# Optimization experiments

Hardware: AMD Instinct MI355X
Metric: run time of the kernel (lower is better)

The kernel has to match this reference:

```python
import jax, jax.numpy as jnp
import numpy as np
from jax import lax

EPS = 1e-5
COMMIT_W = 0.25

def conv2d(x, w, b):
    # x: [N,C,H,W], w: [O,I,3,3], SAME padding, stride 1
    y = lax.conv_general_dilated(x, w, (1, 1), 'SAME',
                                 dimension_numbers=('NCHW', 'OIHW', 'NCHW'))
    return y + b[None, :, None, None]

def batchnorm(x, gamma, beta):
    # training-mode batch norm over (N,H,W)
    m = jnp.mean(x, axis=(0, 2, 3), keepdims=True)
    v = jnp.var(x, axis=(0, 2, 3), keepdims=True)
    xhat = (x - m) * lax.rsqrt(v + EPS)
    return xhat * gamma[None, :, None, None] + beta[None, :, None, None]

def maxpool2(x):
    return lax.reduce_window(x, -jnp.inf, lax.max, (1, 1, 2, 2), (1, 1, 2, 2), 'VALID')

def setup_inputs() -> dict:
    key = jax.random.key(0)
    ks = jax.random.split(key, 8)
    B, C, H, W, D, K = 8, 3, 256, 256, 64, 1024
    return {
        'x': jax.random.normal(ks[0], (B, C, H, W), jnp.float32),
        'conv1_w': jax.random.normal(ks[1], (D, C, 3, 3), jnp.float32) * 0.05,
        'conv1_b': jnp.zeros((D,), jnp.float32),
        'bn1_gamma': jnp.ones((D,), jnp.float32),
        'bn1_beta': jnp.zeros((D,), jnp.float32),
        'embed': jax.random.normal(ks[2], (K, D), jnp.float32),
        'conv2_w': jax.random.normal(ks[3], (C, D, 3, 3), jnp.float32) * 0.05,
        'conv2_b': jnp.zeros((C,), jnp.float32),
        'bn2_gamma': jnp.ones((C,), jnp.float32),
        'bn2_beta': jnp.zeros((C,), jnp.float32),
    }

def reference(x, conv1_w, conv1_b, bn1_gamma, bn1_beta, embed,
              conv2_w, conv2_b, bn2_gamma, bn2_beta):
    # ---- encoder ----
    h = conv2d(x, conv1_w, conv1_b)
    h = batchnorm(h, bn1_gamma, bn1_beta)
    h = jax.nn.relu(h)
    h = maxpool2(h)                      # [B, D, H/2, W/2]
    B, D, Hh, Wh = h.shape
    # ---- vector quantize (accept_image_fmap) ----
    flat = jnp.transpose(h, (0, 2, 3, 1)).reshape(-1, D)   # [N, D]
    # squared euclidean distance to each code
    dist = (jnp.sum(flat * flat, axis=1, keepdims=True)
            - 2.0 * flat @ embed.T
            + jnp.sum(embed * embed, axis=1)[None, :])     # [N, K]
    idx = jnp.argmin(dist, axis=1)                          # [N]
    quant = embed[idx]                                      # gather [N, D]
    commit_loss = COMMIT_W * jnp.mean((lax.stop_gradient(quant) - flat) ** 2)
    # straight-through estimator
    quant_st = flat + lax.stop_gradient(quant - flat)
    q = jnp.transpose(quant_st.reshape(B, Hh, Wh, D), (0, 3, 1, 2))  # [B,D,Hh,Wh]
    indices = idx.reshape(B, Hh, Wh)
    # ---- decoder ----
    up = jnp.repeat(jnp.repeat(q, 2, axis=2), 2, axis=3)    # nearest x2
    y = conv2d(up, conv2_w, conv2_b)
    y = batchnorm(y, bn2_gamma, bn2_beta)
    y = jnp.tanh(y)
    return (y, indices, commit_loss)
```

## Files before the change

### kernel.cpp

```cpp
#include <hip/hip_runtime.h>
#include <hip/hip_bf16.h>
#include <math.h>

typedef unsigned int u32;
typedef unsigned short u16;
typedef __attribute__((ext_vector_type(8))) short short8v;
typedef __attribute__((ext_vector_type(4))) float f32x4;

#define HH 256
#define WW 256
#define HP 128
#define WP 128
#define NPTS (8*HP*WP)
#define NPIX 524288
#define Y_ELEMS (8*3*HH*WW)
#define IDX_OFF Y_ELEMS
#define LOSS_OFF (Y_ELEMS + NPTS)
#define MARGIN_MFMA 0.05f

__device__ __forceinline__ u32 bfr(float f) {
  u32 u = __float_as_uint(f);
  return (u + 0x7FFFu + ((u >> 16) & 1u)) >> 16;
}
__device__ __forceinline__ float bff(u32 h) { return __uint_as_float(h << 16); }

__global__ __launch_bounds__(256) void k1_fused(
    const float* __restrict__ x, const float* __restrict__ w1,
    const float* __restrict__ b1, double* __restrict__ part1,
    float* __restrict__ pooled) {
  __shared__ float wl[27*64];
  __shared__ float b1s[64];
  __shared__ float xs[3][4][68];
  __shared__ double sred[4][128];
  int t = threadIdx.x;
  for (int i = t; i < 27*64; i += 256) { int c = i & 63; int tap = i >> 6; wl[i] = w1[c*27 + tap]; }
  if (t < 64) b1s[t] = b1[t];
  int bx = blockIdx.x;
  int b = bx >> 9;
  int pid0 = (bx & 511) * 32;
  int py = pid0 >> 7;
  int px0 = pid0 & 127;
  int gcol0 = 2*px0 - 1, grow0 = 2*py - 1;
  for (int i = t; i < 816; i += 256) {
    int j = i % 68;
    int rr = (i / 68) & 3;
    int ic = i / 272;
    int col = gcol0 + j, row = grow0 + rr;
    float v = 0.f;
    if (col >= 0 && col < WW && row >= 0 && row < HH)
      v = x[((size_t)((b*3 + ic)*HH + row))*WW + col];
    xs[ic][rr][j] = v;
  }
  __syncthreads();
  int lpx = t >> 3;
  int co = (t & 7) * 8;
  float A0[8], A1[8], C0[8], C1[8];
  #pragma unroll
  for (int c = 0; c < 8; ++c) { float bb = b1s[co + c]; A0[c] = bb; A1[c] = bb; C0[c] = bb; C1[c] = bb; }
  #pragma unroll
  for (int ic = 0; ic < 3; ++ic) {
    #pragma unroll
    for (int dy = 0; dy < 3; ++dy) {
      const float* wb = wl + (size_t)((ic*3 + dy)*3)*64 + co;
      int j0 = 2*lpx;
      float xa0 = xs[ic][dy][j0+0], xa1 = xs[ic][dy][j0+1], xa2 = xs[ic][dy][j0+2], xa3 = xs[ic][dy][j0+3];
      float xc0 = xs[ic][dy+1][j0+0], xc1 = xs[ic][dy+1][j0+1], xc2 = xs[ic][dy+1][j0+2], xc3 = xs[ic][dy+1][j0+3];
      #pragma unroll
      for (int c = 0; c < 8; ++c) {
        float w0 = wb[c], w1v = wb[64 + c], w2v = wb[128 + c];
        A0[c] = fmaf(xa0, w0, fmaf(xa1, w1v, fmaf(xa2, w2v, A0[c])));
        A1[c] = fmaf(xa1, w0, fmaf(xa2, w1v, fmaf(xa3, w2v, A1[c])));
        C0[c] = fmaf(xc0, w0, fmaf(xc1, w1v, fmaf(xc2, w2v, C0[c])));
        C1[c] = fmaf(xc1, w0, fmaf(xc2, w1v, fmaf(xc3, w2v, C1[c])));
      }
    }
  }
  double s[8], q[8];
  float m[8];
  #pragma unroll
  for (int c = 0; c < 8; ++c) {
    double dA0 = (double)A0[c], dA1 = (double)A1[c], dC0 = (double)C0[c], dC1 = (double)C1[c];
    double s_ = 0.0;
    s_ += dA0 + dA1;
    double q_ = fma(dA0, dA0, 0.0);
    q_ = fma(dA1, dA1, q_);
    float m_ = fmaxf(-3.4e38f, fmaxf(A0[c], A1[c]));
    s_ += dC0 + dC1;
    q_ = fma(dC0, dC0, q_);
    q_ = fma(dC1, dC1, q_);
    m_ = fmaxf(m_, fmaxf(C0[c], C1[c]));
    s[c] = s_; q[c] = q_; m[c] = m_;
  }
  int pid = pid0 + lpx;
  size_t p = (size_t)b*16384 + pid;
  *(float4*)(pooled + p*64 + co)     = make_float4(m[0], m[1], m[2], m[3]);
  *(float4*)(pooled + p*64 + co + 4) = make_float4(m[4], m[5], m[6], m[7]);
  #pragma unroll 1
  for (int c = 0; c < 8; ++c) {
    #pragma unroll
    for (int st = 8; st < 64; st <<= 1) {
      s[c] += __shfl_xor(s[c], st, 64);
      q[c] += __shfl_xor(q[c], st, 64);
    }
  }
  int w = t >> 6;
  if ((t & 63) < 8) {
    #pragma unroll
    for (int c = 0; c < 8; ++c) {
      sred[w][co + c] = s[c];
      sred[w][64 + co + c] = q[c];
    }
  }
  __syncthreads();
  if (t < 128)
    part1[(size_t)bx*128 + t] = (sred[0][t] + sred[1][t]) + (sred[2][t] + sred[3][t]);
}

__global__ __launch_bounds__(256) void k2_reduce_bn1(
    const double* __restrict__ part1, const float* __restrict__ gamma,
    const float* __restrict__ beta, double* __restrict__ sAB1,
    const float* __restrict__ w2, float* __restrict__ weff) {
  int bx = blockIdx.x;
  if (bx >= 64) {
    int e = (bx - 64)*256 + threadIdx.x;
    int oc = e & 3;
    int ic = (e >> 2) & 63;
    int combo = e >> 8;
    if (oc == 3) { weff[e] = 0.f; return; }
    int bq = combo & 1, a = (combo >> 1) & 1, ex = (combo >> 2) & 1, ey = combo >> 3;
    int rs = (a == 0) ? 0 : (ey == 0 ? 1 : 2);
    int rc = ((a ^ ey) != 0) ? 2 : 1;
    int cs = (bq == 0) ? 0 : (ex == 0 ? 1 : 2);
    int cc = ((bq ^ ex) != 0) ? 2 : 1;
    float ssum = 0.f;
    for (int i = 0; i < rc; ++i)
      for (int j = 0; j < cc; ++j)
        ssum += w2[((oc*64 + ic)*3 + (rs + i))*3 + (cs + j)];
    weff[e] = ssum;
    return;
  }
  int c = bx, t = threadIdx.x;
  double s = 0.0, q = 0.0;
  for (int i = t; i < 4096; i += 256) {
    const double* p = part1 + (size_t)i*128;
    s += p[c];
    q += p[64 + c];
  }
  __shared__ double ls[256], lq[256];
  ls[t] = s; lq[t] = q;
  __syncthreads();
  for (int o = 128; o > 0; o >>= 1) {
    if (t < o) { ls[t] += ls[t+o]; lq[t] += lq[t+o]; }
    __syncthreads();
  }
  if (t == 0) {
    double mean = ls[0] / (double)NPIX;
    double var  = lq[0] / (double)NPIX - mean*mean;
    double A = (double)gamma[c] / sqrt(var + 1e-5);
    sAB1[c] = A;
    sAB1[64 + c] = (double)beta[c] - mean*A;
  }
}

__global__ void kE_prep(const float* __restrict__ embed, char* __restrict__ epack,
                        double* __restrict__ enormd, float* __restrict__ enf,
                        u32* __restrict__ flagcnt,
                        const float* __restrict__ weff, float* __restrict__ proj) {
  int bxx = blockIdx.x;
  if (bxx >= 4) {
    int e = (bxx - 4)*256 + threadIdx.x;
    int k = e >> 6;
    int slot = e & 63;
    int combo = slot >> 2, oc = slot & 3;
    if (oc == 3) { proj[e] = 0.f; return; }
    const float* er = embed + (size_t)k*64;
    const float* wc = weff + combo*256 + oc;
    float s0 = 0.f, s1 = 0.f;
    #pragma unroll 8
    for (int ic = 0; ic < 64; ic += 2) {
      s0 = fmaf(er[ic],     wc[ic*4],     s0);
      s1 = fmaf(er[ic + 1], wc[ic*4 + 4], s1);
    }
    proj[e] = s0 + s1;
    return;
  }
  if (bxx == 0 && threadIdx.x == 0) flagcnt[0] = 0u;
  int k = bxx*256 + threadIdx.x;
  const float4* e4 = (const float4*)(embed + (size_t)k*64);
  u32 hw[32], lw[32];
  double s0 = 0.0, s1 = 0.0;
  #pragma unroll
  for (int i = 0; i < 16; ++i) {
    float4 v = e4[i];
    float f0 = v.x, f1 = v.y, f2 = v.z, f3 = v.w;
    s0 = fma((double)f0, (double)f0, s0); s1 = fma((double)f1, (double)f1, s1);
    s0 = fma((double)f2, (double)f2, s0); s1 = fma((double)f3, (double)f3, s1);
    u32 h0 = bfr(f0), h1 = bfr(f1), h2 = bfr(f2), h3 = bfr(f3);
    u32 l0 = bfr(f0 - bff(h0)), l1 = bfr(f1 - bff(h1));
    u32 l2 = bfr(f2 - bff(h2)), l3 = bfr(f3 - bff(h3));
    hw[2*i]   = h0 | (h1 << 16);
    hw[2*i+1] = h2 | (h3 << 16);
    lw[2*i]   = l0 | (l1 << 16);
    lw[2*i+1] = l2 | (l3 << 16);
  }
  char* tb = epack + (size_t)(k >> 4)*4096 + (size_t)(k & 15)*16;
  #pragma unroll
  for (int g = 0; g < 4; ++g) {
    *(uint4*)(tb + 0*1024 + g*256) = make_uint4(hw[4*g+0], hw[4*g+1], hw[4*g+2], hw[4*g+3]);
    *(uint4*)(tb + 1*1024 + g*256) = make_uint4(hw[16+4*g+0], hw[16+4*g+1], hw[16+4*g+2], hw[16+4*g+3]);
    *(uint4*)(tb + 2*1024 + g*256) = make_uint4(lw[4*g+0], lw[4*g+1], lw[4*g+2], lw[4*g+3]);
    *(uint4*)(tb + 3*1024 + g*256) = make_uint4(lw[16+4*g+0], lw[16+4*g+1], lw[16+4*g+2], lw[16+4*g+3]);
  }
  double e = s0 + s1;
  enormd[k] = e;
  enf[k] = (float)e;
}

#define MFMA_BF16 __builtin_amdgcn_mfma_f32_16x16x32_bf16
#define PROC_T(ntv) { \
  int code = (ntv)*16 + col; \
  float en2 = senf[code];    \
  f32x4 accA0={en2,en2,en2,en2}, accA1={0.f,0.f,0.f,0.f}; \
  f32x4 accB0={en2,en2,en2,en2}, accB1={0.f,0.f,0.f,0.f}; \
  __builtin_amdgcn_s_setprio(1); \
  accA0 = MFMA_BF16(aA_h0, b_h0, accA0, 0, 0, 0); \
  accA1 = MFMA_BF16(aA_h1, b_h1, accA1, 0, 0, 0); \
  accB0 = MFMA_BF16(aB_h0, b_h0, accB0, 0, 0, 0); \
  accB1 = MFMA_BF16(aB_h1, b_h1, accB1, 0, 0, 0); \
  accA0 = MFMA_BF16(aA_l0, b_h0, accA0, 0, 0, 0); \
  accA1 = MFMA_BF16(aA_l1, b_h1, accA1, 0, 0, 0); \
  accB0 = MFMA_BF16(aB_l0, b_h0, accB0, 0, 0, 0); \
  accB1 = MFMA_BF16(aB_l1, b_h1, accB1, 0, 0, 0); \
  accA0 = MFMA_BF16(aA_h0, b_l0, accA0, 0, 0, 0); \
  accA1 = MFMA_BF16(aA_h1, b_l1, accA1, 0, 0, 0); \
  accB0 = MFMA_BF16(aB_h0, b_l0, accB0, 0, 0, 0); \
  accB1 = MFMA_BF16(aB_h1, b_l1, accB1, 0, 0, 0); \
  __builtin_amdgcn_s_setprio(0); \
  _Pragma("unroll") \
  for (int j = 0; j < 4; ++j) { \
    float mA = accA0[j] + accA1[j]; \
    bool cA = mA > bestA[j]; \
    b2A[j] = __builtin_amdgcn_fmed3f(b2A[j], mA, bestA[j]);   \
    bestA[j] = fmaxf(bestA[j], mA); \
    idxA[j] = cA ? code : idxA[j]; \
    float mB = accB0[j] + accB1[j]; \
    bool cB = mB > bestB[j]; \
    b2B[j] = __builtin_amdgcn_fmed3f(b2B[j], mB, bestB[j]); \
    bestB[j] = fmaxf(bestB[j], mB); \
    idxB[j] = cB ? code : idxB[j]; \
  } \
}
#define PROC_LDS(bb, ntv) { \
  short8v b_h0 = *(const short8v*)((bb) + 0*1024 + lane*16); \
  short8v b_h1 = *(const short8v*)((bb) + 1*1024 + lane*16); \
  short8v b_l0 = *(const short8v*)((bb) + 2*1024 + lane*16); \
  short8v b_l1 = *(const short8v*)((bb) + 3*1024 + lane*16); \
  PROC_T(ntv); \
}

__global__ __launch_bounds__(256) void kB_mfma(
    const float* __restrict__ pooled, const double* __restrict__ sAB1,
    const char* __restrict__ epack, const float* __restrict__ enf,
    int* __restrict__ idxbuf, float* __restrict__ out_f, double* __restrict__ lossq,
    u32* __restrict__ flagcnt, u32* __restrict__ flagids) {
  __shared__ float senf[1024];
  __shared__ char shbuf[32768];
  __shared__ float fnp[256];
  __shared__ float fnsum[128];
  __shared__ float sAs[64], sBs[64];
  __shared__ double wred[4];
  int t = threadIdx.x;
  for (int i = t; i < 1024; i += 256) senf[i] = -0.5f * enf[i];
  if (t < 64) { sAs[t] = (float)sAB1[t]; sBs[t] = (float)sAB1[64 + t]; }
  __syncthreads();
  {
    int lp = t >> 1, h = t & 1, cb = h*32;
    int p = blockIdx.x*128 + lp;
    const float4* src = (const float4*)(pooled + (size_t)p*64 + cb);
    float fn = 0.f;
    u32 hw[16], lw[16];
    #pragma unroll
    for (int i = 0; i < 8; ++i) {
      float4 v = src[i];
      float f0 = fmaxf(fmaf(v.x, sAs[cb+4*i+0], sBs[cb+4*i+0]), 0.f);
      float f1 = fmaxf(fmaf(v.y, sAs[cb+4*i+1], sBs[cb+4*i+1]), 0.f);
      float f2 = fmaxf(fmaf(v.z, sAs[cb+4*i+2], sBs[cb+4*i+2]), 0.f);
      float f3 = fmaxf(fmaf(v.w, sAs[cb+4*i+3], sBs[cb+4*i+3]), 0.f);
      fn = fmaf(f0, f0, fn); fn = fmaf(f1, f1, fn);
      fn = fmaf(f2, f2, fn); fn = fmaf(f3, f3, fn);
      u32 h0 = bfr(f0), h1 = bfr(f1), h2 = bfr(f2), h3 = bfr(f3);
      u32 l0 = bfr(f0 - bff(h0)), l1 = bfr(f1 - bff(h1));
      u32 l2 = bfr(f2 - bff(h2)), l3 = bfr(f3 - bff(h3));
      hw[2*i]   = h0 | (h1 << 16);
      hw[2*i+1] = h2 | (h3 << 16);
      lw[2*i]   = l0 | (l1 << 16);
      lw[2*i+1] = l2 | (l3 << 16);
    }
    uint4* dh = (uint4*)(shbuf + (size_t)lp*256 + h*64);
    uint4* dl = (uint4*)(shbuf + (size_t)lp*256 + 128 + h*64);
    #pragma unroll
    for (int i = 0; i < 4; ++i) dh[i] = make_uint4(hw[4*i], hw[4*i+1], hw[4*i+2], hw[4*i+3]);
    #pragma unroll
    for (int i = 0; i < 4; ++i) dl[i] = make_uint4(lw[4*i], lw[4*i+1], lw[4*i+2], lw[4*i+3]);
    fnp[t] = fn;
  }
  __syncthreads();
  if ((t & 1) == 0) fnsum[t >> 1] = fnp[t] + fnp[t + 1];
  int lane = t & 63;
  int col = lane & 15, g = lane >> 4;
  int w = t >> 6;
  const char* fbA = shbuf + (size_t)(w*32 + col)*256 + 16*g;
  const char* fbB = shbuf + (size_t)(w*32 + 16 + col)*256 + 16*g;
  short8v aA_h0 = *(const short8v*)(fbA);
  short8v aA_h1 = *(const short8v*)(fbA + 64);
  short8v aA_l0 = *(const short8v*)(fbA + 128);
  short8v aA_l1 = *(const short8v*)(fbA + 192);
  short8v aB_h0 = *(const short8v*)(fbB);
  short8v aB_h1 = *(const short8v*)(fbB + 64);
  short8v aB_l0 = *(const short8v*)(fbB + 128);
  short8v aB_l1 = *(const short8v*)(fbB + 192);
  __syncthreads();
  char (*btile)[4][4096] = (char (*)[4][4096])shbuf;
  float bestA[4], b2A[4], bestB[4], b2B[4];
  int idxA[4], idxB[4];
  #pragma unroll
  for (int j = 0; j < 4; ++j) {
    bestA[j] = -3.4e38f; b2A[j] = -3.4e38f; idxA[j] = 0;
    bestB[j] = -3.4e38f; b2B[j] = -3.4e38f; idxB[j] = 0;
  }
  #pragma unroll
  for (int k = 0; k < 4; ++k)
    *(uint4*)(&btile[0][k][t*16]) = *(const uint4*)(epack + (size_t)k*4096 + (size_t)t*16);
  __syncthreads();
  #pragma unroll 1
  for (int ng = 0; ng < 16; ++ng) {
    int cur = ng & 1;
    uint4 stg0, stg1, stg2, stg3;
    if (ng < 15) {
      const char* base = epack + (size_t)(4*ng + 4)*4096 + (size_t)t*16;
      stg0 = *(const uint4*)(base);
      stg1 = *(const uint4*)(base + 4096);
      stg2 = *(const uint4*)(base + 8192);
      stg3 = *(const uint4*)(base + 12288);
    }
    PROC_LDS(&btile[cur][0][0], 4*ng + 0);
    PROC_LDS(&btile[cur][1][0], 4*ng + 1);
    PROC_LDS(&btile[cur][2][0], 4*ng + 2);
    PROC_LDS(&btile[cur][3][0], 4*ng + 3);
    if (ng < 15) {
      *(uint4*)(&btile[cur ^ 1][0][t*16]) = stg0;
      *(uint4*)(&btile[cur ^ 1][1][t*16]) = stg1;
      *(uint4*)(&btile[cur ^ 1][2][t*16]) = stg2;
      *(uint4*)(&btile[cur ^ 1][3][t*16]) = stg3;
    }
    __syncthreads();
  }
  double lsum = 0.0;
  #pragma unroll
  for (int grp = 0; grp < 2; ++grp) {
    #pragma unroll
    for (int j = 0; j < 4; ++j) {
      float b  = (grp == 0) ? bestA[j] : bestB[j];
      float s2 = (grp == 0) ? b2A[j]   : b2B[j];
      int  id  = (grp == 0) ? idxA[j]  : idxB[j];
      #pragma unroll
      for (int m = 1; m < 16; m <<= 1) {
        float ob  = __shfl_xor(b, m, 64);
        float os2 = __shfl_xor(s2, m, 64);
        int  oid  = __shfl_xor(id, m, 64);
        s2 = fmaxf(fmaxf(s2, os2), fminf(b, ob));
        if (ob > b || (ob == b && oid < id)) { b = ob; id = oid; }
      }
      if (col == 0) {
        int lpt = w*32 + grp*16 + g*4 + j;
        int p = blockIdx.x*128 + lpt;
        idxbuf[p] = id;
        out_f[IDX_OFF + p] = (float)id;
        lsum += (double)fmaf(-2.f, b, fnsum[lpt]);
        if (b - s2 <= 0.5f*MARGIN_MFMA) { u32 pos = atomicAdd(flagcnt, 1u); flagids[pos] = (u32)p; }
      }
    }
  }
  #pragma unroll
  for (int m = 1; m < 64; m <<= 1) lsum += __shfl_xor(lsum, m, 64);
  if (lane == 0) wred[w] = lsum;
  __syncthreads();
  if (t == 0) lossq[blockIdx.x] = (wred[0] + wred[1]) + (wred[2] + wred[3]);
}

__global__ __launch_bounds__(64) void kC_fallback(
    const float* __restrict__ x, const float* __restrict__ w1,
    const float* __restrict__ b1, const double* __restrict__ sAB1,
    const float* __restrict__ embed, const double* __restrict__ enormd,
    const u32* __restrict__ flagcnt, const u32* __restrict__ flagids,
    int* __restrict__ idxbuf, float* __restrict__ out_f,
    const double* __restrict__ lossq) {
  int lane = threadIdx.x;
  if (blockIdx.x == gridDim.x - 1) {
    double s = 0.0;
    for (int i = lane; i < 1024; i += 64) s += lossq[i];
    #pragma unroll
    for (int st = 1; st < 64; st <<= 1) s += __shfl_xor(s, st, 64);
    if (lane == 0) out_f[LOSS_OFF] = (float)(0.25 * s / (double)((size_t)NPTS * 64));
    return;
  }
  __shared__ double fd[64];
  double wv[27];
  #pragma unroll
  for (int i = 0; i < 27; ++i) wv[i] = (double)w1[lane*27 + i];
  double bias = (double)b1[lane];
  double A = sAB1[lane], B = sAB1[64 + lane];
  u32 n = flagcnt[0];
  u32 stride = gridDim.x - 1;
  for (u32 i = blockIdx.x; i < n; i += stride) {
    int p = (int)flagids[i];
    int b = p >> 14, py = (p >> 7) & 127, px = p & 127;
    double mx = -1e300;
    #pragma unroll
    for (int ry = 0; ry < 2; ++ry) {
      #pragma unroll
      for (int cx = 0; cx < 2; ++cx) {
        double a = bias;
        int yy = 2*py + ry, xx = 2*px + cx;
        #pragma unroll
        for (int ic = 0; ic < 3; ++ic) {
          #pragma unroll
          for (int dy = 0; dy < 3; ++dy) {
            int ryy = yy + dy - 1;
            if (ryy >= 0 && ryy < HH) {
              const float* row = x + ((size_t)((b*3 + ic)*HH + ryy))*WW;
              #pragma unroll
              for (int dxx = 0; dxx < 3; ++dxx) {
                int xc = xx + dxx - 1;
                if (xc >= 0 && xc < WW) a = fma((double)row[xc], wv[(ic*3 + dy)*3 + dxx], a);
              }
            }
          }
        }
        mx = fmax(mx, a);
      }
    }
    fd[lane] = fmax(fma(mx, A, B), 0.0);
    __syncthreads();
    double bd = 1e300; int bk = 1 << 20;
    for (int kk = 0; kk < 16; ++kk) {
      int k = kk*64 + lane;
      const float* e = embed + (size_t)k*64;
      double e0=0,e1=0,e2=0,e3=0;
      #pragma unroll
      for (int d = 0; d < 16; ++d) {
        e0 = fma(fd[4*d+0], (double)e[4*d+0], e0);
        e1 = fma(fd[4*d+1], (double)e[4*d+1], e1);
        e2 = fma(fd[4*d+2], (double)e[4*d+2], e2);
        e3 = fma(fd[4*d+3], (double)e[4*d+3], e3);
      }
      double dist = fma(-2.0, (e0+e1)+(e2+e3), enormd[k]);
      if (dist < bd) { bd = dist; bk = k; }
    }
    #pragma unroll
    for (int st = 1; st < 64; st <<= 1) {
      double od = __shfl_xor(bd, st, 64);
      int ok = __shfl_xor(bk, st, 64);
      if (od < bd || (od == bd && ok < bk)) { bd = od; bk = ok; }
    }
    if (lane == 0) {
      idxbuf[p] = bk;
      out_f[IDX_OFF + p] = (float)bk;
    }
    __syncthreads();
  }
}

template<int MODE>
__global__ __launch_bounds__(256) void conv2_body(
    const int* __restrict__ idxbuf, const float* __restrict__ proj,
    const float* __restrict__ c2b, const float* __restrict__ sAB2,
    float* __restrict__ part2, float* __restrict__ ybuf, float* __restrict__ yout) {
  __shared__ float xw[4][6];
  int t = threadIdx.x;
  int bx = blockIdx.x;
  int b = bx >> 6;
  int tile = bx & 63;
  int px = (tile & 1)*64 + (t & 63);
  int py = (tile >> 1)*4 + (t >> 6);
  const int* idxb = idxbuf + b*HP*WP;
  float acc[12];
  #pragma unroll
  for (int i = 0; i < 12; ++i) acc[i] = 0.f;
  #pragma unroll
  for (int r = 0; r < 3; ++r) {
    int cy = py - 1 + r;
    bool vy = (cy >= 0) && (cy < HP);
    #pragma unroll
    for (int s = 0; s < 3; ++s) {
      int cx = px - 1 + s;
      if (!(vy && (cx >= 0) && (cx < WP))) continue;
      int ii = idxb[cy*WP + cx];
      const float4* pr = (const float4*)(proj + (size_t)ii*64);
      #pragma unroll
      for (int rp = 0; rp < ((r==1) ? 2 : 1); ++rp) {
        const int pa = (r==0) ? 0 : (r==2) ? 1 : rp;
        const int ca = (r==0) ? 0 : (r==2) ? 1 : (1-rp);
        #pragma unroll
        for (int sp = 0; sp < ((s==1) ? 2 : 1); ++sp) {
          const int pb = (s==0) ? 0 : (s==2) ? 1 : sp;
          const int cb = (s==0) ? 0 : (s==2) ? 1 : (1-sp);
          float4 v = pr[pa*8 + pb*4 + ca*2 + cb];
          int ob = (pa*2 + pb)*3;
          acc[ob+0] += v.x;
          acc[ob+1] += v.y;
          acc[ob+2] += v.z;
        }
      }
    }
  }
  if (MODE == 2) {
    #pragma unroll
    for (int pa = 0; pa < 2; ++pa) {
      int yy = 2*py + pa;
      #pragma unroll
      for (int pb = 0; pb < 2; ++pb) {
        int xx = 2*px + pb;
        int ob = (pa*2 + pb)*3;
        float v0 = tanhf(fmaf(acc[ob+0], sAB2[0], sAB2[4]));
        float v1 = tanhf(fmaf(acc[ob+1], sAB2[1], sAB2[5]));
        float v2 = tanhf(fmaf(acc[ob+2], sAB2[2], sAB2[6]));
        yout[((size_t)(b*3 + 0)*HH + yy)*WW + xx] = v0;
        yout[((size_t)(b*3 + 1)*HH + yy)*WW + xx] = v1;
        yout[((size_t)(b*3 + 2)*HH + yy)*WW + xx] = v2;
      }
    }
  } else {
    float s0=0.f,s1=0.f,s2=0.f, q0=0.f,q1=0.f,q2=0.f;
    #pragma unroll
    for (int pa = 0; pa < 2; ++pa) {
      int yy = 2*py + pa;
      #pragma unroll
      for (int pb = 0; pb < 2; ++pb) {
        int xx = 2*px + pb;
        int ob = (pa*2 + pb)*3;
        float v0 = acc[ob+0] + c2b[0], v1 = acc[ob+1] + c2b[1], v2 = acc[ob+2] + c2b[2];
        s0 += v0; s1 += v1; s2 += v2;
        q0 = fmaf(v0, v0, q0); q1 = fmaf(v1, v1, q1); q2 = fmaf(v2, v2, q2);
        if (MODE == 1) {
          ybuf[((size_t)(b*3 + 0)*HH + yy)*WW + xx] = v0;
          ybuf[((size_t)(b*3 + 1)*HH + yy)*WW + xx] = v1;
          ybuf[((size_t)(b*3 + 2)*HH + yy)*WW + xx] = v2;
        }
      }
    }
    float sv[3] = {s0, s1, s2}, qv2[3] = {q0, q1, q2};
    #pragma unroll
    for (int oc = 0; oc < 3; ++oc) {
      float v = sv[oc], q = qv2[oc];
      #pragma unroll
      for (int m = 1; m < 64; m <<= 1) { v += __shfl_xor(v, m, 64); q += __shfl_xor(q, m, 64); }
      if ((t & 63) == 0) { xw[t >> 6][oc] = v; xw[t >> 6][3 + oc] = q; }
    }
    __syncthreads();
    if (t == 0) {
      #pragma unroll
      for (int i = 0; i < 6; ++i)
        part2[bx*6 + i] = (xw[0][i] + xw[1][i]) + (xw[2][i] + xw[3][i]);
    }
  }
}

__global__ __launch_bounds__(256) void k7_reduce_bn2(
    const float* __restrict__ part2, const float* __restrict__ g2,
    const float* __restrict__ bt2, const float* __restrict__ c2b,
    float* __restrict__ sAB2, int fold_bias) {
  int t = threadIdx.x;
  int w = t >> 6, lane = t & 63;
  if (w >= 3) return;
  double s = 0.0, q = 0.0;
  for (int i = lane; i < 512; i += 64) {
    s += (double)part2[i*6 + w];
    q += (double)part2[i*6 + 3 + w];
  }
  #pragma unroll
  for (int m = 1; m < 64; m <<= 1) { s += __shfl_xor(s, m, 64); q += __shfl_xor(q, m, 64); }
  if (lane == 0) {
    double mean = s / (double)NPIX;
    double var  = q / (double)NPIX - mean*mean;
    double A = (double)g2[w] / sqrt(var + 1e-5);
    double Bc = (double)bt2[w] - mean*A;
    if (fold_bias) Bc += (double)c2b[w]*A;
    sAB2[w] = (float)A;
    sAB2[4 + w] = (float)Bc;
  }
}

__global__ __launch_bounds__(256) void k8_apply(
    const float* __restrict__ ybuf, const float* __restrict__ sAB2,
    float* __restrict__ yout) {
  int i4 = blockIdx.x*256 + threadIdx.x;
  int i = i4 * 4;
  int oc = (i >> 16) % 3;
  float A = sAB2[oc], B = sAB2[4 + oc];
  float4 v = *(const float4*)(ybuf + i);
  float4 r;
  r.x = tanhf(fmaf(v.x, A, B));
  r.y = tanhf(fmaf(v.y, A, B));
  r.z = tanhf(fmaf(v.z, A, B));
  r.w = tanhf(fmaf(v.w, A, B));
  *(float4*)(yout + i) = r;
}

extern "C" void kernel_launch(void* const* d_in, const int* in_sizes, int n_in,
                              void* d_out, int out_size, void* d_ws, size_t ws_size,
                              hipStream_t stream) {
  const float* x   = (const float*)d_in[0];
  const float* w1  = (const float*)d_in[1];
  const float* b1  = (const float*)d_in[2];
  const float* g1  = (const float*)d_in[3];
  const float* bt1 = (const float*)d_in[4];
  const float* emb = (const float*)d_in[5];
  const float* w2  = (const float*)d_in[6];
  const float* b2  = (const float*)d_in[7];
  const float* g2  = (const float*)d_in[8];
  const float* bt2 = (const float*)d_in[9];
  float* out = (float*)d_out;

  char* ws = (char*)d_ws;
  float*  pooled  = (float*) (ws);
  double* part1   = (double*)(ws + 33554432);
  char*   epack   =          (ws + 33554432);
  float*  proj    = (float*) (ws + 33816576);
  int*    idxbuf  = (int*)   (ws + 37748736);
  u32*    flagids = (u32*)   (ws + 38273024);
  u32*    flagcnt = (u32*)   (ws + 38797312);
  float*  part2   = (float*) (ws + 38799424);
  double* sAB1    = (double*)(ws + 38811712);
  float*  sAB2    = (float*) (ws + 38812736);
  double* enormd  = (double*)(ws + 38812800);
  float*  enf     = (float*) (ws + 38820992);
  float*  weff    = (float*) (ws + 38825088);
  double* lossq   = (double*)(ws + 38841472);
  float*  ybuf    = (float*) (ws + 38849664);
  bool use_ybuf = (ws_size >= (size_t)45141120);

  hipLaunchKernelGGL(k1_fused, dim3(4096), dim3(256), 0, stream, x, w1, b1, part1, pooled);
  hipLaunchKernelGGL(k2_reduce_bn1, dim3(80), dim3(256), 0, stream, part1, g1, bt1, sAB1, w2, weff);
  hipLaunchKernelGGL(kE_prep, dim3(260), dim3(256), 0, stream, emb, epack, enormd, enf, flagcnt, weff, proj);
  hipLaunchKernelGGL(kB_mfma, dim3(1024), dim3(256), 0, stream, pooled, sAB1, (const char*)epack,
                     enf, idxbuf, out, lossq, flagcnt, flagids);
  hipLaunchKernelGGL(kC_fallback, dim3(2049), dim3(64), 0, stream, x, w1, b1, sAB1, emb, enormd,
                     flagcnt, flagids, idxbuf, out, lossq);
  if (use_ybuf) {
    hipLaunchKernelGGL((conv2_body<1>), dim3(512), dim3(256), 0, stream, idxbuf, proj, b2, sAB2, part2, ybuf, out);
    hipLaunchKernelGGL(k7_reduce_bn2, dim3(1), dim3(256), 0, stream, part2, g2, bt2, b2, sAB2, 0);
    hipLaunchKernelGGL(k8_apply, dim3(1536), dim3(256), 0, stream, ybuf, sAB2, out);
  } else {
    hipLaunchKernelGGL((conv2_body<0>), dim3(512), dim3(256), 0, stream, idxbuf, proj, b2, sAB2, part2, ybuf, out);
    hipLaunchKernelGGL(k7_reduce_bn2, dim3(1), dim3(256), 0, stream, part2, g2, bt2, b2, sAB2, 1);
    hipLaunchKernelGGL((conv2_body<2>), dim3(512), dim3(256), 0, stream, idxbuf, proj, b2, sAB2, part2, ybuf, out);
  }
}
```

Before: 200.7 us.

## Use float BN1 partial stats in conv1 and fold BN2 reduce into apply

The conv1 epilogue now computes per-channel sums, sums of squares and the cross-lane shuffle reductions in float instead of double, converting to double only when writing to shared memory. The separate single-block BN2 reduction kernel is removed, and every block of the apply kernel recomputes the BN2 scale and shift from the partials itself. This cuts FP64 work and shuffle traffic in conv1 and saves one kernel launch and its serial gap. In exchange, BN1 statistics lose some precision and each of the 1536 apply blocks repeats the small 512-entry reduction.

```diff
diff --git a/kernel.cpp b/kernel.cpp
--- a/kernel.cpp
+++ b/kernel.cpp
@@ -75,21 +75,17 @@
       }
     }
   }
-  double s[8], q[8];
-  float m[8];
+  float fs[8], fq[8], m[8];
   #pragma unroll
   for (int c = 0; c < 8; ++c) {
-    double dA0 = (double)A0[c], dA1 = (double)A1[c], dC0 = (double)C0[c], dC1 = (double)C1[c];
-    double s_ = 0.0;
-    s_ += dA0 + dA1;
-    double q_ = fma(dA0, dA0, 0.0);
-    q_ = fma(dA1, dA1, q_);
-    float m_ = fmaxf(-3.4e38f, fmaxf(A0[c], A1[c]));
-    s_ += dC0 + dC1;
-    q_ = fma(dC0, dC0, q_);
-    q_ = fma(dC1, dC1, q_);
-    m_ = fmaxf(m_, fmaxf(C0[c], C1[c]));
-    s[c] = s_; q[c] = q_; m[c] = m_;
+    float a0 = A0[c], a1 = A1[c], c0 = C0[c], c1 = C1[c];
+    fs[c] = (a0 + a1) + (c0 + c1);
+    float q_ = fmaf(a0, a0, 0.f);
+    q_ = fmaf(a1, a1, q_);
+    q_ = fmaf(c0, c0, q_);
+    q_ = fmaf(c1, c1, q_);
+    fq[c] = q_;
+    m[c] = fmaxf(fmaxf(a0, a1), fmaxf(c0, c1));
   }
   int pid = pid0 + lpx;
   size_t p = (size_t)b*16384 + pid;
@@ -99,16 +95,16 @@
   for (int c = 0; c < 8; ++c) {
     #pragma unroll
     for (int st = 8; st < 64; st <<= 1) {
-      s[c] += __shfl_xor(s[c], st, 64);
-      q[c] += __shfl_xor(q[c], st, 64);
+      fs[c] += __shfl_xor(fs[c], st, 64);
+      fq[c] += __shfl_xor(fq[c], st, 64);
     }
   }
   int w = t >> 6;
   if ((t & 63) < 8) {
     #pragma unroll
     for (int c = 0; c < 8; ++c) {
-      sred[w][co + c] = s[c];
-      sred[w][64 + co + c] = q[c];
+      sred[w][co + c] = (double)fs[c];
+      sred[w][64 + co + c] = (double)fq[c];
     }
   }
   __syncthreads();
@@ -592,12 +588,33 @@
 }
 
 __global__ __launch_bounds__(256) void k8_apply(
-    const float* __restrict__ ybuf, const float* __restrict__ sAB2,
+    const float* __restrict__ part2, const float* __restrict__ g2,
+    const float* __restrict__ bt2, const float* __restrict__ ybuf,
     float* __restrict__ yout) {
-  int i4 = blockIdx.x*256 + threadIdx.x;
+  __shared__ float sab[8];
+  int t = threadIdx.x;
+  int w = t >> 6, lane = t & 63;
+  if (w < 3) {
+    double s = 0.0, q = 0.0;
+    for (int i = lane; i < 512; i += 64) {
+      s += (double)part2[i*6 + w];
+      q += (double)part2[i*6 + 3 + w];
+    }
+    #pragma unroll
+    for (int m = 1; m < 64; m <<= 1) { s += __shfl_xor(s, m, 64); q += __shfl_xor(q, m, 64); }
+    if (lane == 0) {
+      double mean = s / (double)NPIX;
+      double var  = q / (double)NPIX - mean*mean;
+      double A = (double)g2[w] / sqrt(var + 1e-5);
+      sab[w] = (float)A;
+      sab[4 + w] = (float)((double)bt2[w] - mean*A);
+    }
+  }
+  __syncthreads();
+  int i4 = blockIdx.x*256 + t;
   int i = i4 * 4;
   int oc = (i >> 16) % 3;
-  float A = sAB2[oc], B = sAB2[4 + oc];
+  float A = sab[oc], B = sab[4 + oc];
   float4 v = *(const float4*)(ybuf + i);
   float4 r;
   r.x = tanhf(fmaf(v.x, A, B));
@@ -649,8 +666,7 @@
                      flagcnt, flagids, idxbuf, out, lossq);
   if (use_ybuf) {
     hipLaunchKernelGGL((conv2_body<1>), dim3(512), dim3(256), 0, stream, idxbuf, proj, b2, sAB2, part2, ybuf, out);
-    hipLaunchKernelGGL(k7_reduce_bn2, dim3(1), dim3(256), 0, stream, part2, g2, bt2, b2, sAB2, 0);
-    hipLaunchKernelGGL(k8_apply, dim3(1536), dim3(256), 0, stream, ybuf, sAB2, out);
+    hipLaunchKernelGGL(k8_apply, dim3(1536), dim3(256), 0, stream, part2, g2, bt2, ybuf, out);
   } else {
     hipLaunchKernelGGL((conv2_body<0>), dim3(512), dim3(256), 0, stream, idxbuf, proj, b2, sAB2, part2, ybuf, out);
     hipLaunchKernelGGL(k7_reduce_bn2, dim3(1), dim3(256), 0, stream, part2, g2, bt2, b2, sAB2, 1);
```

After: 203.5 us. No clear change (+1.4%).
